# Performance work log

Hardware: AMD Instinct MI355X
Metric: run time of the kernel (lower is better)

## Reference

```python
import jax, jax.numpy as jnp
import numpy as np

H = 8  # heads, hard-coded in the original module


def setup_inputs() -> dict:
    key = jax.random.key(0)
    ks = jax.random.split(key, 7)
    B, Lq, Lkv = 4, 2048, 512
    dim_q, dim_kv = 1024, 768
    q = jax.random.normal(ks[0], (B, Lq, dim_q), dtype=jnp.float32)
    kv = jax.random.normal(ks[1], (B, Lkv, dim_kv), dtype=jnp.float32)
    # Linear weights stored as [in, out] so y = x @ W (math-equivalent to torch Linear)
    Wq = jax.random.normal(ks[2], (dim_q, dim_q), dtype=jnp.float32) / np.sqrt(dim_q)
    Wk = jax.random.normal(ks[3], (dim_kv, dim_q), dtype=jnp.float32) / np.sqrt(dim_kv)
    Wv = jax.random.normal(ks[4], (dim_kv, dim_q), dtype=jnp.float32) / np.sqrt(dim_kv)
    Wo = jax.random.normal(ks[5], (dim_q, dim_q), dtype=jnp.float32) / np.sqrt(dim_q)
    bo = jax.random.normal(ks[6], (dim_q,), dtype=jnp.float32) * 0.01
    return {"q": q, "kv": kv, "Wq": Wq, "Wk": Wk, "Wv": Wv, "Wo": Wo, "bo": bo}


def reference(q, kv, Wq, Wk, Wv, Wo, bo):
    B, Lq, dim_q = q.shape
    hd = dim_q // H
    scale = jnp.asarray(hd, q.dtype) ** -0.5
    # projections
    qp = q @ Wq   # [B, Lq, dim_q]
    kp = kv @ Wk  # [B, Lkv, dim_q]
    vp = kv @ Wv  # [B, Lkv, dim_q]
    # split heads: [B, L, H, hd]
    qh = qp.reshape(B, Lq, H, hd)
    kh = kp.reshape(B, kv.shape[1], H, hd)
    vh = vp.reshape(B, kv.shape[1], H, hd)
    # scaled attention scores and softmax
    scores = jnp.einsum("bqhd,bkhd->bhqk", qh, kh) * scale
    attn = jax.nn.softmax(scores, axis=-1)
    out = jnp.einsum("bhqk,bkhd->bqhd", attn, vh).reshape(B, Lq, dim_q)
    return out @ Wo + bo
```

## Files before the change

### kernel.cpp

```cpp
#include <hip/hip_runtime.h>
#include <hip/hip_cooperative_groups.h>

namespace cg = cooperative_groups;


typedef unsigned short u16;
typedef unsigned int u32;
using short8  = __attribute__((ext_vector_type(8))) short;
using floatx4 = __attribute__((ext_vector_type(4))) float;

__device__ inline u16 f2bf(float x) {
  union { float f; u32 u; } v; v.f = x;
  u32 r = (v.u + 0x7fffu + ((v.u >> 16) & 1u)) >> 16;
  return (u16)r;
}

__device__ inline float fast_exp2(float x) {
#if __has_builtin(__builtin_amdgcn_exp2f)
  return __builtin_amdgcn_exp2f(x);
#else
  return exp2f(x);
#endif
}

#define MFMA(a, b, c) __builtin_amdgcn_mfma_f32_16x16x32_bf16(a, b, c, 0, 0, 0)

__device__ inline void async_lds16(const void* g, void* l) {
  __builtin_amdgcn_global_load_lds(
      (const __attribute__((address_space(1))) void*)g,
      (__attribute__((address_space(3))) void*)l, 16, 0, 0);
}

__global__ void cvt_all(const float* __restrict__ q, const float* __restrict__ kv,
                        u16* __restrict__ q_bf, u16* __restrict__ kv_bf) {
  int i = blockIdx.x * 256 + threadIdx.x;
  const float* src; u16* dst; int idx;
  if (i < 1048576) { src = q;  dst = q_bf;  idx = i; }
  else             { src = kv; dst = kv_bf; idx = i - 1048576; }
  float4 a = ((const float4*)src)[2 * idx];
  float4 b = ((const float4*)src)[2 * idx + 1];
  u16 t[8] = {f2bf(a.x), f2bf(a.y), f2bf(a.z), f2bf(a.w),
              f2bf(b.x), f2bf(b.y), f2bf(b.z), f2bf(b.w)};
  ((short8*)dst)[idx] = *(short8*)t;
}

__global__ __launch_bounds__(256)
void transpose_all(const float* __restrict__ Wq, const float* __restrict__ Wk,
                   const float* __restrict__ Wv, const float* __restrict__ Wo,
                   u16* __restrict__ WqT, u16* __restrict__ WkvT, u16* __restrict__ WoT) {
  __shared__ float tile[64][68];
  const int z = blockIdx.z;
  const float* W; u16* Wt; int K;
  if      (z == 0) { W = Wq; Wt = WqT;               K = 1024; }
  else if (z == 1) { W = Wk; Wt = WkvT;              K = 768;  }
  else if (z == 2) { W = Wv; Wt = WkvT + 1024 * 768; K = 768;  }
  else             { W = Wo; Wt = WoT;               K = 1024; }
  const int k0 = blockIdx.y * 64, n0 = blockIdx.x * 64;
  if (k0 >= K) return;
  const int N = 1024;
  const int t = threadIdx.x;
  for (int p = 0; p < 4; ++p) {
    int cid = p * 256 + t;
    int row = cid >> 4, c = cid & 15;
    float4 v = *(const float4*)&W[(long)(k0 + row) * N + n0 + c * 4];
    tile[row][c * 4 + 0] = v.x; tile[row][c * 4 + 1] = v.y;
    tile[row][c * 4 + 2] = v.z; tile[row][c * 4 + 3] = v.w;
  }
  __syncthreads();
  for (int p = 0; p < 2; ++p) {
    int oc = p * 256 + t;
    int n = oc >> 3, c = oc & 7;
    u16 tmp[8];
    for (int s = 0; s < 8; ++s) tmp[s] = f2bf(tile[c * 8 + s][n]);
    *(short8*)&Wt[(long)(n0 + n) * K + k0 + c * 8] = *(short8*)tmp;
  }
}

__device__ __forceinline__
void gemm_body(const u16* __restrict__ A, const u16* __restrict__ Bt,
               u16* __restrict__ Cb, float* __restrict__ Cf,
               const float* __restrict__ bias, u16* __restrict__ vt_out,
               int K, int ldc, int lin, int mt_per_xcd, u16* smem) {
  u16* As = smem;
  u16* Bs = smem + 8192;
  const int tid  = threadIdx.x;
  const int wave = tid >> 6, lane = tid & 63;
  const int l15  = lane & 15, quad = lane >> 4;
  const int wm   = (wave >> 1) * 64, wn = (wave & 1) * 64;
  const int xcd  = lin & 7, slot = lin >> 3;
  const int mt   = xcd * mt_per_xcd + (slot % mt_per_xcd);
  const int nti  = slot / mt_per_xcd;
  const long m0  = (long)mt * 128, n0 = (long)nti * 128;
  const int lrow = lane >> 3;
  const int lk   = (lane & 7) * 8;

  floatx4 acc[4][4] = {};

  for (int k0 = 0; k0 < K; k0 += 64) {
    for (int c = 0; c < 4; ++c) {
      int rbase = (wave * 4 + c) * 8;
      async_lds16(A  + (m0 + rbase + lrow) * (long)K + k0 + lk, &As[(wave * 4 + c) * 512]);
      async_lds16(Bt + (n0 + rbase + lrow) * (long)K + k0 + lk, &Bs[(wave * 4 + c) * 512]);
    }
    __syncthreads();
    for (int kc = 0; kc < 2; ++kc) {
      short8 af[4], bfr[4];
      for (int i = 0; i < 4; ++i)
        af[i] = *(const short8*)&As[(wm + i * 16 + l15) * 64 + kc * 32 + quad * 8];
      for (int j = 0; j < 4; ++j)
        bfr[j] = *(const short8*)&Bs[(wn + j * 16 + l15) * 64 + kc * 32 + quad * 8];
      for (int i = 0; i < 4; ++i)
        for (int j = 0; j < 4; ++j)
          acc[i][j] = MFMA(af[i], bfr[j], acc[i][j]);
    }
    __syncthreads();
  }

  if (Cf) {
    for (int i = 0; i < 4; ++i)
      for (int j = 0; j < 4; ++j) {
        long row = m0 + wm + i * 16 + quad * 4;
        long col = n0 + wn + j * 16 + l15;
        float b = bias ? bias[col] : 0.f;
        for (int r = 0; r < 4; ++r) Cf[(row + r) * (long)ldc + col] = acc[i][j][r] + b;
      }
    return;
  }
  for (int i = 0; i < 4; ++i)
    for (int j = 0; j < 4; ++j)
      for (int r = 0; r < 4; ++r)
        smem[(wm + i * 16 + quad * 4 + r) * 138 + wn + j * 16 + l15] = f2bf(acc[i][j][r]);
  __syncthreads();
  if (vt_out && nti >= 8) {
    const int h  = nti - 8;
    const int bq = (int)(m0 >> 9);
    const int l0 = (int)(m0 & 511);
    u16* vbase = vt_out + ((long)(bq * 8 + h) * 128) * 512;
    for (int p = 0; p < 8; ++p) {
      int cid = p * 256 + tid;
      int d = cid >> 4, c = cid & 15;
      u16 tmp[8];
      for (int s = 0; s < 8; ++s) tmp[s] = smem[(c * 8 + s) * 138 + d];
      *(short8*)&vbase[(long)d * 512 + l0 + c * 8] = *(short8*)tmp;
    }
  } else {
    for (int p = 0; p < 8; ++p) {
      int cid = p * 256 + tid;
      int row = cid >> 4, c = cid & 15;
      short8 v = *(const short8*)&smem[row * 138 + c * 8];
      *(short8*)&Cb[(m0 + row) * (long)ldc + n0 + c * 8] = v;
    }
  }
}

__device__ __forceinline__
void attn_body(const u16* __restrict__ qp, const u16* __restrict__ kp,
               const u16* __restrict__ vT, u16* __restrict__ ctx,
               int lin, u16* smem) {
  u16* Ks = smem;
  u16* Vs = smem + 8192;
  const int tid  = threadIdx.x;
  const int wave = tid >> 6, lane = tid & 63;
  u16* Pw = smem + 16384 + wave * 1024;
  const int l15  = lane & 15, quad = lane >> 4;
  const int xcd  = lin & 7, slot = lin >> 3;
  const int pairIdx = xcd * 4 + (slot & 3);
  const int b = pairIdx >> 3, h = pairIdx & 7;
  const int qtile = slot >> 2;
  const long rowbase = (long)b * 2048 + qtile * 64 + wave * 16;
  const float sc = 0.08838834764831845f * 1.4426950408889634f;

  short8 aQ[4];
  for (int dc = 0; dc < 4; ++dc)
    aQ[dc] = *(const short8*)&qp[(rowbase + l15) * 1024 + h * 128 + dc * 32 + quad * 8];

  floatx4 O[8] = {};
  float lsum[4] = {};
  const u16* kpb   = kp + ((long)b * 512) * 1024 + h * 128;
  const u16* vbase = vT + ((long)(b * 8 + h) * 128) * 512;

  const int krow = lane >> 4;
  const int kpos = lane & 15;
  const int vrow = lane >> 3;
  const int vpos = lane & 7;

  for (int t = 0; t < 8; ++t) {
    for (int i = 0; i < 4; ++i) {
      int inst = wave * 4 + i;
      int row  = inst * 4 + krow;
      int g    = kpos ^ (row & 15);
      async_lds16(kpb + (long)(t * 64 + row) * 1024 + g * 8, &Ks[inst * 512]);
    }
    for (int i = 0; i < 4; ++i) {
      int inst = wave * 4 + i;
      int d    = inst * 8 + vrow;
      int g    = vpos ^ (d & 7);
      async_lds16(vbase + (long)d * 512 + t * 64 + g * 8, &Vs[inst * 512]);
    }
    __syncthreads();

    floatx4 S[4] = {};
    for (int dc = 0; dc < 4; ++dc)
      for (int ks = 0; ks < 4; ++ks) {
        int k = ks * 16 + l15;
        short8 bk = *(const short8*)&Ks[k * 128 + (((dc * 4 + quad) ^ l15) * 8)];
        S[ks] = MFMA(aQ[dc], bk, S[ks]);
      }
    for (int ks = 0; ks < 4; ++ks)
      for (int r = 0; r < 4; ++r) {
        float p = fast_exp2(S[ks][r] * sc);
        lsum[r] += p;
        int row = quad * 4 + r;
        int g   = (ks * 2 + (l15 >> 3)) ^ (row & 7);
        Pw[row * 64 + g * 8 + (l15 & 7)] = f2bf(p);
      }
    short8 aP[2];
    for (int kc = 0; kc < 2; ++kc)
      aP[kc] = *(const short8*)&Pw[l15 * 64 + (((kc * 4 + quad) ^ (l15 & 7)) * 8)];
    for (int j = 0; j < 8; ++j) {
      int d = j * 16 + l15;
      short8 bV0 = *(const short8*)&Vs[d * 64 + ((quad ^ (l15 & 7)) * 8)];
      short8 bV1 = *(const short8*)&Vs[d * 64 + (((4 + quad) ^ (l15 & 7)) * 8)];
      O[j] = MFMA(aP[0], bV0, O[j]);
      O[j] = MFMA(aP[1], bV1, O[j]);
    }
    __syncthreads();
  }

  for (int r = 0; r < 4; ++r) {
    float sum = lsum[r];
    for (int off = 1; off < 16; off <<= 1) sum += __shfl_xor(sum, off);
    lsum[r] = 1.f / sum;
  }
  for (int j = 0; j < 8; ++j)
    for (int r = 0; r < 4; ++r)
      ctx[(rowbase + quad * 4 + r) * 1024 + h * 128 + j * 16 + l15] =
          f2bf(O[j][r] * lsum[r]);
}

__global__ __launch_bounds__(256, 4)
void mega(const u16* q_bf, const u16* WqT, const u16* kv_bf, const u16* WkvT,
          const u16* WoT, u16* qp, u16* kp, u16* vT, u16* ctx,
          float* out, const float* bo) {
  __shared__ u16 smem[20480];
  cg::grid_group g = cg::this_grid();
  const int bid = blockIdx.x;

  if (bid < 768) {
    const bool isQ = bid < 512;
    gemm_body(isQ ? q_bf : kv_bf, isQ ? WqT : WkvT, isQ ? qp : kp,
              nullptr, nullptr, isQ ? (u16*)nullptr : vT,
              isQ ? 1024 : 768, 1024, isQ ? bid : bid - 512, isQ ? 8 : 2, smem);
  }
  g.sync();
  attn_body(qp, kp, vT, ctx, bid, smem);
  g.sync();
  if (bid < 512)
    gemm_body(ctx, WoT, nullptr, out, bo, nullptr, 1024, 1024, bid, 8, smem);
}

__global__ __launch_bounds__(256)
void k_proj_q(const u16* __restrict__ q_bf, const u16* __restrict__ WqT,
              u16* __restrict__ qp) {
  __shared__ u16 smem[17664];
  gemm_body(q_bf, WqT, qp, nullptr, nullptr, nullptr, 1024, 1024, blockIdx.x, 8, smem);
}
__global__ __launch_bounds__(256)
void k_proj_kv(const u16* __restrict__ kv_bf, const u16* __restrict__ WkvT,
               u16* __restrict__ kp, u16* __restrict__ vT) {
  __shared__ u16 smem[17664];
  gemm_body(kv_bf, WkvT, kp, nullptr, nullptr, vT, 768, 1024, blockIdx.x, 2, smem);
}
__global__ __launch_bounds__(256, 4)
void k_attn(const u16* __restrict__ qp, const u16* __restrict__ kp,
            const u16* __restrict__ vT, u16* __restrict__ ctx) {
  __shared__ u16 smem[20480];
  attn_body(qp, kp, vT, ctx, blockIdx.x, smem);
}
__global__ __launch_bounds__(256)
void k_oproj(const u16* __restrict__ ctx, const u16* __restrict__ WoT,
             float* __restrict__ out, const float* __restrict__ bo) {
  __shared__ u16 smem[17664];
  gemm_body(ctx, WoT, nullptr, out, bo, nullptr, 1024, 1024, blockIdx.x, 8, smem);
}

extern "C" void kernel_launch(void* const* d_in, const int* in_sizes, int n_in,
                              void* d_out, int out_size, void* d_ws, size_t ws_size,
                              hipStream_t stream) {
  const float* q  = (const float*)d_in[0];
  const float* kv = (const float*)d_in[1];
  const float* Wq = (const float*)d_in[2];
  const float* Wk = (const float*)d_in[3];
  const float* Wv = (const float*)d_in[4];
  const float* Wo = (const float*)d_in[5];
  const float* bo = (const float*)d_in[6];
  float* out = (float*)d_out;

  char* ws = (char*)d_ws;
  u16* q_bf  = (u16*)(ws + 0);
  u16* kv_bf = (u16*)(ws + 16777216);
  u16* WqT   = (u16*)(ws + 19922944);
  u16* WkvT  = (u16*)(ws + 22020096);
  u16* WoT   = (u16*)(ws + 25165824);
  u16* qp    = (u16*)(ws + 27262976);
  u16* kp    = (u16*)(ws + 44040192);
  u16* vT    = (u16*)(ws + 52428800);
  u16* ctx   = (u16*)(ws + 56623104);

  cvt_all<<<4864, 256, 0, stream>>>(q, kv, q_bf, kv_bf);
  transpose_all<<<dim3(16, 16, 4), 256, 0, stream>>>(Wq, Wk, Wv, Wo, WqT, WkvT, WoT);

  int maxb = 0;
  hipError_t oe = hipOccupancyMaxActiveBlocksPerMultiprocessor(
      &maxb, (const void*)mega, 256, 0);
  if (oe == hipSuccess && maxb >= 4) {
    void* args[] = {(void*)&q_bf, (void*)&WqT, (void*)&kv_bf, (void*)&WkvT,
                    (void*)&WoT, (void*)&qp, (void*)&kp, (void*)&vT,
                    (void*)&ctx, (void*)&out, (void*)&bo};
    hipLaunchCooperativeKernel((const void*)mega, dim3(1024), dim3(256),
                               args, 0, stream);
  } else {
    k_proj_q<<<512, 256, 0, stream>>>(q_bf, WqT, qp);
    k_proj_kv<<<256, 256, 0, stream>>>(kv_bf, WkvT, kp, vT);
    k_attn<<<1024, 256, 0, stream>>>(qp, kp, vT, ctx);
    k_oproj<<<512, 256, 0, stream>>>(ctx, WoT, out, bo);
  }
}
```

Measured before the change: 211.2 us.

## Replace grid-wide barriers with per-tile dataflow flags in cooperative megakernel

The two cooperative grid.sync barriers are replaced by fine-grained per-tile ready flags in global memory. Q and KV projection tiles publish release flags, attention blocks spin-wait only on the Q/K/V tiles they need, and output-projection blocks wait only on their own attention tiles. The flags are zeroed in the conversion kernel. This lets stages overlap instead of draining the whole grid at each phase boundary, at the cost of spin polling and reliance on the tile-to-block mapping and co-residency being correct.

```diff
diff --git a/kernel.cpp b/kernel.cpp
--- a/kernel.cpp
+++ b/kernel.cpp
@@ -1,7 +1,4 @@
 #include <hip/hip_runtime.h>
-#include <hip/hip_cooperative_groups.h>
-
-namespace cg = cooperative_groups;
 
 
 typedef unsigned short u16;
@@ -31,9 +28,21 @@
       (__attribute__((address_space(3))) void*)l, 16, 0, 0);
 }
 
+__device__ inline void spin_wait(volatile u32* p) {
+  while (__hip_atomic_load((const u32*)p, __ATOMIC_RELAXED,
+                           __HIP_MEMORY_SCOPE_AGENT) == 0u)
+    __builtin_amdgcn_s_sleep(2);
+}
+__device__ inline void flag_set(u32* p) {
+  __hip_atomic_store(p, 1u, __ATOMIC_RELEASE, __HIP_MEMORY_SCOPE_AGENT);
+}
+
 __global__ void cvt_all(const float* __restrict__ q, const float* __restrict__ kv,
-                        u16* __restrict__ q_bf, u16* __restrict__ kv_bf) {
+                        u16* __restrict__ q_bf, u16* __restrict__ kv_bf,
+                        u32* __restrict__ flags) {
   int i = blockIdx.x * 256 + threadIdx.x;
+  if (blockIdx.x == 0)
+    for (int j = threadIdx.x; j < 1792; j += 256) flags[j] = 0;
   const float* src; u16* dst; int idx;
   if (i < 1048576) { src = q;  dst = q_bf;  idx = i; }
   else             { src = kv; dst = kv_bf; idx = i - 1048576; }
@@ -241,22 +250,54 @@
 __global__ __launch_bounds__(256, 4)
 void mega(const u16* q_bf, const u16* WqT, const u16* kv_bf, const u16* WkvT,
           const u16* WoT, u16* qp, u16* kp, u16* vT, u16* ctx,
-          float* out, const float* bo) {
+          float* out, const float* bo,
+          u32* qflag, u32* kvflag, u32* aflag) {
   __shared__ u16 smem[20480];
-  cg::grid_group g = cg::this_grid();
   const int bid = blockIdx.x;
-
-  if (bid < 768) {
-    const bool isQ = bid < 512;
-    gemm_body(isQ ? q_bf : kv_bf, isQ ? WqT : WkvT, isQ ? qp : kp,
-              nullptr, nullptr, isQ ? (u16*)nullptr : vT,
-              isQ ? 1024 : 768, 1024, isQ ? bid : bid - 512, isQ ? 8 : 2, smem);
-  }
-  g.sync();
-  attn_body(qp, kp, vT, ctx, bid, smem);
-  g.sync();
-  if (bid < 512)
+  const int tid = threadIdx.x;
+
+  if (bid < 512) {
+    gemm_body(q_bf, WqT, qp, nullptr, nullptr, nullptr, 1024, 1024, bid, 8, smem);
+    int xcd = bid & 7, slot = bid >> 3;
+    int mt = xcd * 8 + (slot & 7), nti = slot >> 3;
+    __threadfence(); __syncthreads();
+    if (tid == 0) flag_set(&qflag[mt * 8 + nti]);
+  } else if (bid < 768) {
+    int lin = bid - 512;
+    gemm_body(kv_bf, WkvT, kp, nullptr, nullptr, vT, 768, 1024, lin, 2, smem);
+    int xcd = lin & 7, slot = lin >> 3;
+    int mt = xcd * 2 + (slot & 1), nti = slot >> 1;
+    __threadfence(); __syncthreads();
+    if (tid == 0) flag_set(&kvflag[mt * 16 + nti]);
+  }
+
+  {
+    int xcd = bid & 7, slot = bid >> 3;
+    int pairIdx = xcd * 4 + (slot & 3);
+    int b = pairIdx >> 3, h = pairIdx & 7;
+    int qtile = slot >> 2;
+    if (tid == 0)                    spin_wait(&qflag[(b * 16 + (qtile >> 1)) * 8 + h]);
+    if (tid >= 32 && tid < 36)       spin_wait(&kvflag[(b * 4 + (tid - 32)) * 16 + h]);
+    if (tid >= 64 && tid < 68)       spin_wait(&kvflag[(b * 4 + (tid - 64)) * 16 + 8 + h]);
+    __syncthreads();
+    __threadfence();
+    attn_body(qp, kp, vT, ctx, bid, smem);
+    __threadfence(); __syncthreads();
+    if (tid == 0) flag_set(&aflag[pairIdx * 32 + qtile]);
+  }
+
+  if (bid < 512) {
+    int xcd = bid & 7, slot = bid >> 3;
+    int mt = xcd * 8 + (slot & 7);
+    int b = mt >> 4, qt0 = (mt & 15) * 2;
+    if (tid < 16) {
+      int h = tid >> 1, qt = qt0 + (tid & 1);
+      spin_wait(&aflag[(b * 8 + h) * 32 + qt]);
+    }
+    __syncthreads();
+    __threadfence();
     gemm_body(ctx, WoT, nullptr, out, bo, nullptr, 1024, 1024, bid, 8, smem);
+  }
 }
 
 __global__ __launch_bounds__(256)
@@ -306,8 +347,12 @@
   u16* kp    = (u16*)(ws + 44040192);
   u16* vT    = (u16*)(ws + 52428800);
   u16* ctx   = (u16*)(ws + 56623104);
-
-  cvt_all<<<4864, 256, 0, stream>>>(q, kv, q_bf, kv_bf);
+  u32* flags = (u32*)(ws + 73400320);
+  u32* qflag  = flags;
+  u32* kvflag = flags + 512;
+  u32* aflag  = flags + 768;
+
+  cvt_all<<<4864, 256, 0, stream>>>(q, kv, q_bf, kv_bf, flags);
   transpose_all<<<dim3(16, 16, 4), 256, 0, stream>>>(Wq, Wk, Wv, Wo, WqT, WkvT, WoT);
 
   int maxb = 0;
@@ -316,7 +361,8 @@
   if (oe == hipSuccess && maxb >= 4) {
     void* args[] = {(void*)&q_bf, (void*)&WqT, (void*)&kv_bf, (void*)&WkvT,
                     (void*)&WoT, (void*)&qp, (void*)&kp, (void*)&vT,
-                    (void*)&ctx, (void*)&out, (void*)&bo};
+                    (void*)&ctx, (void*)&out, (void*)&bo,
+                    (void*)&qflag, (void*)&kvflag, (void*)&aflag};
     hipLaunchCooperativeKernel((const void*)mega, dim3(1024), dim3(256),
                                args, 0, stream);
   } else {
```

Result: no change. 212.9 us (+0.8%).
